# Kernel tuning notes

Measured on AMD Instinct MI355X. Metric: run time of the kernel, lower is better.

## Reference

```python
import jax, jax.numpy as jnp
import numpy as np

EPS = 1e-05  # matches module EPS buffer

def setup_inputs() -> dict:
    key = jax.random.key(0)
    ks = jax.random.split(key, 7)
    B, IN, OUT = 1024, 4096, 4096
    init_log_std = np.log(0.0005).astype(np.float32)
    return {
        "x": jax.random.normal(ks[0], (B, IN), dtype=jnp.float32),
        "weight_mean": jax.random.normal(ks[1], (OUT, IN), dtype=jnp.float32) * (IN ** -0.5),
        "weight_std_param": jnp.full((OUT, IN), init_log_std, dtype=jnp.float32) + 0.01 * jax.random.normal(ks[2], (OUT, IN), dtype=jnp.float32),
        "bias_mean": jax.random.normal(ks[3], (OUT,), dtype=jnp.float32) * (IN ** -0.5),
        "bias_std_param": jnp.full((OUT,), init_log_std, dtype=jnp.float32) + 0.01 * jax.random.normal(ks[4], (OUT,), dtype=jnp.float32),
        "noise_w": jax.random.normal(ks[5], (OUT, IN), dtype=jnp.float32),
        "noise_b": jax.random.normal(ks[6], (OUT,), dtype=jnp.float32),
    }

def reference(x, weight_mean, weight_std_param, bias_mean, bias_std_param, noise_w, noise_b):
    # weight_std = clamp(exp(param), min=EPS); sample = mean + noise * std
    w_std = jnp.maximum(jnp.exp(weight_std_param), EPS)
    b_std = jnp.maximum(jnp.exp(bias_std_param), EPS)
    weight = weight_mean + noise_w * w_std          # [OUT, IN]
    bias = bias_mean + noise_b * b_std              # [OUT]
    # F.linear: x @ weight.T + bias
    return jnp.einsum("bi,oi->bo", x, weight) + bias
```

## Files before the change

### kernel.cpp

```cpp
#include <hip/hip_runtime.h>
#include <stdint.h>

#define EPS 1e-5f

typedef short bf16x8 __attribute__((ext_vector_type(8)));
typedef float f32x4 __attribute__((ext_vector_type(4)));

constexpr int M = 1024, N = 4096, K = 4096;
constexpr int BM = 64, BN = 128, BK = 64;
constexpr int NTK = K / BK;

constexpr int PREP_BLOCKS = 2048;
constexpr int64_t W4 = (int64_t)N * K / 4;
constexpr int64_t X4 = (int64_t)M * K / 4;
constexpr int W4_PER_BLK = (int)(W4 / PREP_BLOCKS);
constexpr int X4_PER_BLK = (int)(X4 / PREP_BLOCKS);
static_assert(W4 % PREP_BLOCKS == 0 && X4 % PREP_BLOCKS == 0, "divide");

__device__ __forceinline__ unsigned short f2bf(float f) {
  union { float f; uint32_t u; } v; v.f = f;
  uint32_t r = (v.u + 0x7fffu + ((v.u >> 16) & 1u)) >> 16;
  return (unsigned short)r;
}

__device__ __forceinline__ void gload16(const void* g, void* l) {
  __builtin_amdgcn_global_load_lds(
      (const __attribute__((address_space(1))) void*)(uintptr_t)g,
      (__attribute__((address_space(3))) void*)(uintptr_t)l, 16, 0, 0);
}

__device__ __forceinline__ void cvt8(const f32x4& a0, const f32x4& a1,
                                     const f32x4& s0, const f32x4& s1,
                                     const f32x4& n0, const f32x4& n1,
                                     bf16x8& o) {
  o[0] = (short)f2bf(a0[0] + n0[0] * fmaxf(__expf(s0[0]), EPS));
  o[1] = (short)f2bf(a0[1] + n0[1] * fmaxf(__expf(s0[1]), EPS));
  o[2] = (short)f2bf(a0[2] + n0[2] * fmaxf(__expf(s0[2]), EPS));
  o[3] = (short)f2bf(a0[3] + n0[3] * fmaxf(__expf(s0[3]), EPS));
  o[4] = (short)f2bf(a1[0] + n1[0] * fmaxf(__expf(s1[0]), EPS));
  o[5] = (short)f2bf(a1[1] + n1[1] * fmaxf(__expf(s1[1]), EPS));
  o[6] = (short)f2bf(a1[2] + n1[2] * fmaxf(__expf(s1[2]), EPS));
  o[7] = (short)f2bf(a1[3] + n1[3] * fmaxf(__expf(s1[3]), EPS));
}

__global__ __launch_bounds__(256) void prep_kernel(
    const float* __restrict__ wm, const float* __restrict__ wsp,
    const float* __restrict__ nw, const float* __restrict__ bm,
    const float* __restrict__ bsp, const float* __restrict__ nb,
    const float* __restrict__ x,
    unsigned short* __restrict__ w_bf, unsigned short* __restrict__ x_bf,
    float* __restrict__ bias)
{
  const int tid = threadIdx.x;
  const int bid = blockIdx.x;
  const f32x4* wm4  = (const f32x4*)wm;
  const f32x4* wsp4 = (const f32x4*)wsp;
  const f32x4* nw4  = (const f32x4*)nw;
  const f32x4* x4   = (const f32x4*)x;
  bf16x8* wb8 = (bf16x8*)w_bf;
  bf16x8* xb8 = (bf16x8*)x_bf;

  {
    const int64_t base4 = (int64_t)bid * W4_PER_BLK;
    const int64_t base8 = base4 >> 1;
#pragma unroll
    for (int it = 0; it < 4; ++it) {
      const int p = it * 256 + tid;
      const int64_t i = base4 + (int64_t)p * 2;
      f32x4 a0 = wm4[i],  a1 = wm4[i + 1];
      f32x4 s0 = wsp4[i], s1 = wsp4[i + 1];
      f32x4 n0 = nw4[i],  n1 = nw4[i + 1];
      bf16x8 o;
      cvt8(a0, a1, s0, s1, n0, n1, o);
      wb8[base8 + p] = o;
    }
  }

  {
    const int64_t base4 = (int64_t)bid * X4_PER_BLK;
    const int64_t i = base4 + (int64_t)tid * 2;
    f32x4 v0 = x4[i], v1 = x4[i + 1];
    bf16x8 o;
    o[0] = (short)f2bf(v0[0]); o[1] = (short)f2bf(v0[1]);
    o[2] = (short)f2bf(v0[2]); o[3] = (short)f2bf(v0[3]);
    o[4] = (short)f2bf(v1[0]); o[5] = (short)f2bf(v1[1]);
    o[6] = (short)f2bf(v1[2]); o[7] = (short)f2bf(v1[3]);
    xb8[(base4 >> 1) + tid] = o;
  }

  const int64_t gt = (int64_t)bid * 256 + tid;
  if (gt < N / 4) {
    float4 a = ((const float4*)bm)[gt];
    float4 s = ((const float4*)bsp)[gt];
    float4 n = ((const float4*)nb)[gt];
    float4 o;
    o.x = a.x + n.x * fmaxf(__expf(s.x), EPS);
    o.y = a.y + n.y * fmaxf(__expf(s.y), EPS);
    o.z = a.z + n.z * fmaxf(__expf(s.z), EPS);
    o.w = a.w + n.w * fmaxf(__expf(s.w), EPS);
    ((float4*)bias)[gt] = o;
  }
}

__global__ __launch_bounds__(256) void gemm_kernel(
    const unsigned short* __restrict__ Abf,
    const unsigned short* __restrict__ Bbf,
    const float* __restrict__ bias,
    float* __restrict__ out)
{
  __shared__ unsigned short lds_mem[2][(BM + BN) * BK];

  const int nwg = gridDim.x;
  const int bid = blockIdx.x;
  const int lid = (bid % 8) * (nwg / 8) + bid / 8;
  const int bc = lid >> 4;
  const int br = lid & 15;

  const int tid = threadIdx.x;
  const int lane = tid & 63;
  const int wid = tid >> 6;

  const int srow = wid * 8 + (lane >> 3);
  const int scol = (((lane & 7) ^ (lane >> 3)) * 8);
  const unsigned short* gA = Abf + (int64_t)(br * BM + srow) * K + scol;
  const unsigned short* gB = Bbf + (int64_t)(bc * BN + srow) * K + scol;

  unsigned short* ldsA0 = &lds_mem[0][0];
  unsigned short* ldsB0 = &lds_mem[0][BM * BK];
  unsigned short* ldsA1 = &lds_mem[1][0];
  unsigned short* ldsB1 = &lds_mem[1][BM * BK];
  const int woff = wid * 8 * BK;

  auto stage = [&](int b, int t) {
    const unsigned short* ga = gA + t * BK;
    const unsigned short* gb = gB + t * BK;
    unsigned short* la = (b ? ldsA1 : ldsA0) + woff;
    unsigned short* lb = (b ? ldsB1 : ldsB0) + woff;
    gload16(ga,          la);
    gload16(ga + 32 * K, la + 32 * BK);
    gload16(gb,          lb);
    gload16(gb + 32 * K, lb + 32 * BK);
    gload16(gb + 64 * K, lb + 64 * BK);
    gload16(gb + 96 * K, lb + 96 * BK);
  };

  f32x4 acc[2][4] = {};
  const int fr = lane & 15;
  const int hi = lane >> 4;
  const int rl = lane & 7;
  const int c0 = ((hi ^ rl) << 3);
  const int c1 = (((4 + hi) ^ rl) << 3);
  const int am = (wid >> 1) * 32;
  const int an = (wid & 1) * 64;

  stage(0, 0);

  int cur = 0;
  for (int t = 0; t < NTK; ++t) {
    __syncthreads();
    if (t + 1 < NTK) stage(cur ^ 1, t + 1);
    const unsigned short* lA = cur ? ldsA1 : ldsA0;
    const unsigned short* lB = cur ? ldsB1 : ldsB0;
#pragma unroll
    for (int kk = 0; kk < 2; ++kk) {
      const int c = kk ? c1 : c0;
      bf16x8 a0 = *(const bf16x8*)&lA[(am +  0 + fr) * BK + c];
      bf16x8 a1 = *(const bf16x8*)&lA[(am + 16 + fr) * BK + c];
      bf16x8 b0 = *(const bf16x8*)&lB[(an +  0 + fr) * BK + c];
      bf16x8 b1 = *(const bf16x8*)&lB[(an + 16 + fr) * BK + c];
      bf16x8 b2 = *(const bf16x8*)&lB[(an + 32 + fr) * BK + c];
      bf16x8 b3 = *(const bf16x8*)&lB[(an + 48 + fr) * BK + c];
      acc[0][0] = __builtin_amdgcn_mfma_f32_16x16x32_bf16(a0, b0, acc[0][0], 0, 0, 0);
      acc[0][1] = __builtin_amdgcn_mfma_f32_16x16x32_bf16(a0, b1, acc[0][1], 0, 0, 0);
      acc[0][2] = __builtin_amdgcn_mfma_f32_16x16x32_bf16(a0, b2, acc[0][2], 0, 0, 0);
      acc[0][3] = __builtin_amdgcn_mfma_f32_16x16x32_bf16(a0, b3, acc[0][3], 0, 0, 0);
      acc[1][0] = __builtin_amdgcn_mfma_f32_16x16x32_bf16(a1, b0, acc[1][0], 0, 0, 0);
      acc[1][1] = __builtin_amdgcn_mfma_f32_16x16x32_bf16(a1, b1, acc[1][1], 0, 0, 0);
      acc[1][2] = __builtin_amdgcn_mfma_f32_16x16x32_bf16(a1, b2, acc[1][2], 0, 0, 0);
      acc[1][3] = __builtin_amdgcn_mfma_f32_16x16x32_bf16(a1, b3, acc[1][3], 0, 0, 0);
    }
    cur ^= 1;
  }

  const int orow0 = br * BM + am + (lane >> 4) * 4;
  const int ocol0 = bc * BN + an + fr;
#pragma unroll
  for (int i = 0; i < 2; ++i) {
#pragma unroll
    for (int j = 0; j < 4; ++j) {
      const int col = ocol0 + j * 16;
      const float bv = bias[col];
      const int row = orow0 + i * 16;
#pragma unroll
      for (int r = 0; r < 4; ++r)
        out[(int64_t)(row + r) * N + col] = acc[i][j][r] + bv;
    }
  }
}

__global__ __launch_bounds__(256) void fallback_kernel(
    const float* __restrict__ x, const float* __restrict__ wm,
    const float* __restrict__ wsp, const float* __restrict__ bm,
    const float* __restrict__ bsp, const float* __restrict__ nw,
    const float* __restrict__ nb, float* __restrict__ out)
{
  int64_t idx = (int64_t)blockIdx.x * 256 + threadIdx.x;
  if (idx >= (int64_t)M * N) return;
  int b = (int)(idx >> 12);
  int o = (int)(idx & (N - 1));
  const float* xr = x + (int64_t)b * K;
  const float* wmr = wm + (int64_t)o * K;
  const float* wsr = wsp + (int64_t)o * K;
  const float* nwr = nw + (int64_t)o * K;
  float s = 0.f;
  for (int k = 0; k < K; ++k)
    s += xr[k] * (wmr[k] + nwr[k] * fmaxf(__expf(wsr[k]), EPS));
  out[idx] = s + bm[o] + nb[o] * fmaxf(__expf(bsp[o]), EPS);
}

extern "C" void kernel_launch(void* const* d_in, const int* in_sizes, int n_in,
                              void* d_out, int out_size, void* d_ws, size_t ws_size,
                              hipStream_t stream) {
  const float* x   = (const float*)d_in[0];
  const float* wm  = (const float*)d_in[1];
  const float* wsp = (const float*)d_in[2];
  const float* bm  = (const float*)d_in[3];
  const float* bsp = (const float*)d_in[4];
  const float* nw  = (const float*)d_in[5];
  const float* nb  = (const float*)d_in[6];
  float* out = (float*)d_out;

  const size_t w_bytes = (size_t)N * K * 2;
  const size_t x_bytes = (size_t)M * K * 2;
  const size_t b_bytes = (size_t)N * 4;
  if (ws_size < w_bytes + x_bytes + b_bytes) {
    fallback_kernel<<<(int)(((int64_t)M * N + 255) / 256), 256, 0, stream>>>(
        x, wm, wsp, bm, bsp, nw, nb, out);
    return;
  }

  char* ws = (char*)d_ws;
  unsigned short* w_bf = (unsigned short*)ws;
  unsigned short* x_bf = (unsigned short*)(ws + w_bytes);
  float* bias = (float*)(ws + w_bytes + x_bytes);

  prep_kernel<<<PREP_BLOCKS, 256, 0, stream>>>(wm, wsp, nw, bm, bsp, nb, x, w_bf, x_bf, bias);
  gemm_kernel<<<(M / BM) * (N / BN), 256, 0, stream>>>(x_bf, w_bf, bias, out);
}
```

Before: 84.03 us.

## Load A operand directly from global into registers, keep only B in LDS

The GEMM no longer stages the activation (A) tile through shared memory. Each wave loads its A fragments straight from global memory into registers, double-buffered across two k-steps, while B keeps the async global-to-LDS path. This is meant to cut LDS capacity and LDS traffic per block, which may allow higher occupancy. The cost is uncoalesced-ish 16-byte global loads for A, duplicated across the waves that share rows, and more registers held per thread.

```diff
diff --git a/kernel.cpp b/kernel.cpp
--- a/kernel.cpp
+++ b/kernel.cpp
@@ -9,6 +9,7 @@
 constexpr int M = 1024, N = 4096, K = 4096;
 constexpr int BM = 64, BN = 128, BK = 64;
 constexpr int NTK = K / BK;
+constexpr int GEMM_GRID = (M / BM) * (N / BN);
 
 constexpr int PREP_BLOCKS = 2048;
 constexpr int64_t W4 = (int64_t)N * K / 4;
@@ -75,7 +76,6 @@
       wb8[base8 + p] = o;
     }
   }
-
   {
     const int64_t base4 = (int64_t)bid * X4_PER_BLK;
     const int64_t i = base4 + (int64_t)tid * 2;
@@ -87,7 +87,6 @@
     o[6] = (short)f2bf(v1[2]); o[7] = (short)f2bf(v1[3]);
     xb8[(base4 >> 1) + tid] = o;
   }
-
   const int64_t gt = (int64_t)bid * 256 + tid;
   if (gt < N / 4) {
     float4 a = ((const float4*)bm)[gt];
@@ -108,7 +107,7 @@
     const float* __restrict__ bias,
     float* __restrict__ out)
 {
-  __shared__ unsigned short lds_mem[2][(BM + BN) * BK];
+  __shared__ unsigned short ldsB[2][BN * BK];
 
   const int nwg = gridDim.x;
   const int bid = blockIdx.x;
@@ -121,23 +120,13 @@
   const int wid = tid >> 6;
 
   const int srow = wid * 8 + (lane >> 3);
-  const int scol = (((lane & 7) ^ (lane >> 3)) * 8);
-  const unsigned short* gA = Abf + (int64_t)(br * BM + srow) * K + scol;
+  const int scol = ((lane & 7) ^ (lane >> 3)) * 8;
   const unsigned short* gB = Bbf + (int64_t)(bc * BN + srow) * K + scol;
-
-  unsigned short* ldsA0 = &lds_mem[0][0];
-  unsigned short* ldsB0 = &lds_mem[0][BM * BK];
-  unsigned short* ldsA1 = &lds_mem[1][0];
-  unsigned short* ldsB1 = &lds_mem[1][BM * BK];
   const int woff = wid * 8 * BK;
 
-  auto stage = [&](int b, int t) {
-    const unsigned short* ga = gA + t * BK;
+  auto stageB = [&](int b, int t) {
     const unsigned short* gb = gB + t * BK;
-    unsigned short* la = (b ? ldsA1 : ldsA0) + woff;
-    unsigned short* lb = (b ? ldsB1 : ldsB0) + woff;
-    gload16(ga,          la);
-    gload16(ga + 32 * K, la + 32 * BK);
+    unsigned short* lb = &ldsB[b][0] + woff;
     gload16(gb,          lb);
     gload16(gb + 32 * K, lb + 32 * BK);
     gload16(gb + 64 * K, lb + 64 * BK);
@@ -153,43 +142,61 @@
   const int am = (wid >> 1) * 32;
   const int an = (wid & 1) * 64;
 
-  stage(0, 0);
+  const unsigned short* gAf = Abf + (int64_t)(br * BM + am + fr) * K + hi * 8;
+
+  auto loadA = [&](int t, bf16x8 A[2][2]) {
+#pragma unroll
+    for (int i = 0; i < 2; ++i)
+#pragma unroll
+      for (int kk = 0; kk < 2; ++kk)
+        A[i][kk] = *(const bf16x8*)&gAf[(int64_t)16 * i * K + t * BK + kk * 32];
+  };
+
+  bf16x8 aA[2][2], aB[2][2];
+  loadA(0, aA);
+  stageB(0, 0);
 
   int cur = 0;
-  for (int t = 0; t < NTK; ++t) {
+  auto kstep = [&](int t, bf16x8 Ac[2][2], bf16x8 An[2][2]) {
     __syncthreads();
-    if (t + 1 < NTK) stage(cur ^ 1, t + 1);
-    const unsigned short* lA = cur ? ldsA1 : ldsA0;
-    const unsigned short* lB = cur ? ldsB1 : ldsB0;
+    if (t + 1 < NTK) {
+      stageB(cur ^ 1, t + 1);
+      loadA(t + 1, An);
+    }
+    const unsigned short* lB = &ldsB[cur][0];
 #pragma unroll
     for (int kk = 0; kk < 2; ++kk) {
       const int c = kk ? c1 : c0;
-      bf16x8 a0 = *(const bf16x8*)&lA[(am +  0 + fr) * BK + c];
-      bf16x8 a1 = *(const bf16x8*)&lA[(am + 16 + fr) * BK + c];
       bf16x8 b0 = *(const bf16x8*)&lB[(an +  0 + fr) * BK + c];
       bf16x8 b1 = *(const bf16x8*)&lB[(an + 16 + fr) * BK + c];
       bf16x8 b2 = *(const bf16x8*)&lB[(an + 32 + fr) * BK + c];
       bf16x8 b3 = *(const bf16x8*)&lB[(an + 48 + fr) * BK + c];
-      acc[0][0] = __builtin_amdgcn_mfma_f32_16x16x32_bf16(a0, b0, acc[0][0], 0, 0, 0);
-      acc[0][1] = __builtin_amdgcn_mfma_f32_16x16x32_bf16(a0, b1, acc[0][1], 0, 0, 0);
-      acc[0][2] = __builtin_amdgcn_mfma_f32_16x16x32_bf16(a0, b2, acc[0][2], 0, 0, 0);
-      acc[0][3] = __builtin_amdgcn_mfma_f32_16x16x32_bf16(a0, b3, acc[0][3], 0, 0, 0);
-      acc[1][0] = __builtin_amdgcn_mfma_f32_16x16x32_bf16(a1, b0, acc[1][0], 0, 0, 0);
-      acc[1][1] = __builtin_amdgcn_mfma_f32_16x16x32_bf16(a1, b1, acc[1][1], 0, 0, 0);
-      acc[1][2] = __builtin_amdgcn_mfma_f32_16x16x32_bf16(a1, b2, acc[1][2], 0, 0, 0);
-      acc[1][3] = __builtin_amdgcn_mfma_f32_16x16x32_bf16(a1, b3, acc[1][3], 0, 0, 0);
+      acc[0][0] = __builtin_amdgcn_mfma_f32_16x16x32_bf16(Ac[0][kk], b0, acc[0][0], 0, 0, 0);
+      acc[0][1] = __builtin_amdgcn_mfma_f32_16x16x32_bf16(Ac[0][kk], b1, acc[0][1], 0, 0, 0);
+      acc[0][2] = __builtin_amdgcn_mfma_f32_16x16x32_bf16(Ac[0][kk], b2, acc[0][2], 0, 0, 0);
+      acc[0][3] = __builtin_amdgcn_mfma_f32_16x16x32_bf16(Ac[0][kk], b3, acc[0][3], 0, 0, 0);
+      acc[1][0] = __builtin_amdgcn_mfma_f32_16x16x32_bf16(Ac[1][kk], b0, acc[1][0], 0, 0, 0);
+      acc[1][1] = __builtin_amdgcn_mfma_f32_16x16x32_bf16(Ac[1][kk], b1, acc[1][1], 0, 0, 0);
+      acc[1][2] = __builtin_amdgcn_mfma_f32_16x16x32_bf16(Ac[1][kk], b2, acc[1][2], 0, 0, 0);
+      acc[1][3] = __builtin_amdgcn_mfma_f32_16x16x32_bf16(Ac[1][kk], b3, acc[1][3], 0, 0, 0);
     }
     cur ^= 1;
-  }
-
-  const int orow0 = br * BM + am + (lane >> 4) * 4;
+  };
+
+  static_assert(NTK % 2 == 0, "2-step unroll");
+  for (int t = 0; t < NTK; t += 2) {
+    kstep(t,     aA, aB);
+    kstep(t + 1, aB, aA);
+  }
+
+  const int orow0 = br * BM + am + hi * 4;
   const int ocol0 = bc * BN + an + fr;
 #pragma unroll
-  for (int i = 0; i < 2; ++i) {
-#pragma unroll
-    for (int j = 0; j < 4; ++j) {
-      const int col = ocol0 + j * 16;
-      const float bv = bias[col];
+  for (int j = 0; j < 4; ++j) {
+    const int col = ocol0 + j * 16;
+    const float bv = bias[col];
+#pragma unroll
+    for (int i = 0; i < 2; ++i) {
       const int row = orow0 + i * 16;
 #pragma unroll
       for (int r = 0; r < 4; ++r)
@@ -245,5 +252,5 @@
   float* bias = (float*)(ws + w_bytes + x_bytes);
 
   prep_kernel<<<PREP_BLOCKS, 256, 0, stream>>>(wm, wsp, nw, bm, bsp, nb, x, w_bf, x_bf, bias);
-  gemm_kernel<<<(M / BM) * (N / BN), 256, 0, stream>>>(x_bf, w_bf, bias, out);
-}
+  gemm_kernel<<<GEMM_GRID, 256, 0, stream>>>(x_bf, w_bf, bias, out);
+}
```

Result: slower. 129.2 us (+53.8%).
